# Performance work log

Hardware: AMD Instinct MI355X
Metric: run time of the kernel (lower is better)

## Reference

```python
import jax, jax.numpy as jnp
import numpy as np

N_NODES = 4096
N_EDGES = 16384
D_IN = 128
HID = 1024


def _linear_params(key, fan_in, fan_out):
    kw, kb = jax.random.split(key)
    bound = 1.0 / np.sqrt(fan_in)
    W = jax.random.uniform(kw, (fan_in, fan_out), jnp.float32, -bound, bound)
    b = jax.random.uniform(kb, (fan_out,), jnp.float32, -bound, bound)
    return W, b


def setup_inputs() -> dict:
    key = jax.random.key(0)
    ks = jax.random.split(key, 10)
    H = jax.random.normal(ks[0], (N_NODES, D_IN), jnp.float32)
    e = jax.random.uniform(ks[1], (N_NODES,), jnp.float32)
    # true incidence matrices: one-hot source/destination node per edge
    src = jax.random.randint(ks[2], (N_EDGES,), 0, N_NODES)
    dst = jax.random.randint(ks[3], (N_EDGES,), 0, N_NODES)
    Ro = jax.nn.one_hot(src, N_NODES, dtype=jnp.float32)  # [E, N]
    Ri = jax.nn.one_hot(dst, N_NODES, dtype=jnp.float32)  # [E, N]
    W1, b1 = _linear_params(ks[4], 3 * D_IN, HID)
    W2, b2 = _linear_params(ks[5], HID, HID)
    W3, b3 = _linear_params(ks[6], HID, HID // 2)
    W4, b4 = _linear_params(ks[7], HID // 2, HID // 4)
    W5, b5 = _linear_params(ks[8], HID // 4, 1)
    return {"H": H, "Ro": Ro, "Ri": Ri, "e": e,
            "W1": W1, "b1": b1, "W2": W2, "b2": b2, "W3": W3, "b3": b3,
            "W4": W4, "b4": b4, "W5": W5, "b5": b5}


def reference(H, Ro, Ri, e, W1, b1, W2, b2, W3, b3, W4, b4, W5, b5):
    eH = e[:, None] * H                      # [N, D]
    Ho = Ri.T @ (Ro @ eH)                    # aggregate over edges -> [N, D]
    Hi = Ro.T @ (Ri @ eH)                    # [N, D]
    x = jnp.concatenate([Ho, H, Hi], axis=1)  # [N, 3D]
    x = jnp.tanh(x @ W1 + b1)
    x = jnp.tanh(x @ W2 + b2)
    x = jnp.tanh(x @ W3 + b3)
    x = jnp.tanh(x @ W4 + b4)
    return jax.nn.sigmoid(x @ W5 + b5)       # [N, 1]
```

## Files before the change

kernel.cpp:

```cpp
#include <hip/hip_runtime.h>
#include <hip/hip_bf16.h>
#include <math.h>

#define N_NODES 4096
#define N_EDGES 16384
#define D_IN 128
#define HID 1024

typedef short s8v __attribute__((ext_vector_type(8)));
typedef float f4v __attribute__((ext_vector_type(4)));

__device__ __forceinline__ unsigned short f2b(float v) {
    union { float f; unsigned int u; } c; c.f = v;
    unsigned int u = c.u + 0x7fffu + ((c.u >> 16) & 1u);
    return (unsigned short)(u >> 16);
}
__device__ __forceinline__ float b2f(unsigned short b) {
    union { unsigned int u; float f; } c; c.u = ((unsigned int)b) << 16;
    return c.f;
}
__device__ __forceinline__ void glds16(const unsigned short* g, unsigned short* l) {
    __builtin_amdgcn_global_load_lds(
        (const __attribute__((address_space(1))) void*)g,
        (__attribute__((address_space(3))) void*)l, 16, 0, 0);
}

__global__ void extract_scatter(const float* __restrict__ Ro, const float* __restrict__ Ri,
                                const float* __restrict__ H, const float* __restrict__ e,
                                float* __restrict__ xf) {
    int edge = (blockIdx.x * 256 + threadIdx.x) >> 6;
    int l = threadIdx.x & 63;
    const float4* ro4 = (const float4*)(Ro + (size_t)edge * N_NODES);
    const float4* ri4 = (const float4*)(Ri + (size_t)edge * N_NODES);
    int src = -1, dst = -1;
    for (int it = 0; it < 16; ++it) {
        if (src < 0) {
            float4 v = ro4[it * 64 + l];
            bool hit = (v.x != 0.0f) | (v.y != 0.0f) | (v.z != 0.0f) | (v.w != 0.0f);
            unsigned long long m = __ballot(hit);
            if (m) {
                int fl = __ffsll((long long)m) - 1;
                int idx = 0;
                if (hit) idx = (it * 64 + l) * 4 + (v.x != 0.0f ? 0 : v.y != 0.0f ? 1 : v.z != 0.0f ? 2 : 3);
                src = __shfl(idx, fl);
            }
        }
        if (dst < 0) {
            float4 v = ri4[it * 64 + l];
            bool hit = (v.x != 0.0f) | (v.y != 0.0f) | (v.z != 0.0f) | (v.w != 0.0f);
            unsigned long long m = __ballot(hit);
            if (m) {
                int fl = __ffsll((long long)m) - 1;
                int idx = 0;
                if (hit) idx = (it * 64 + l) * 4 + (v.x != 0.0f ? 0 : v.y != 0.0f ? 1 : v.z != 0.0f ? 2 : 3);
                dst = __shfl(idx, fl);
            }
        }
        if (src >= 0 && dst >= 0) break;
    }
    float es = e[src], ed = e[dst];
    if (l < 32) {
        int f = l * 4;
        float4 h = *(const float4*)(H + (size_t)src * 128 + f);
        float* o = xf + (size_t)dst * 256 + f;
        atomicAdd(o + 0, es * h.x); atomicAdd(o + 1, es * h.y);
        atomicAdd(o + 2, es * h.z); atomicAdd(o + 3, es * h.w);
    } else {
        int f = (l - 32) * 4;
        float4 h = *(const float4*)(H + (size_t)dst * 128 + f);
        float* o = xf + (size_t)src * 256 + 128 + f;
        atomicAdd(o + 0, ed * h.x); atomicAdd(o + 1, ed * h.y);
        atomicAdd(o + 2, ed * h.z); atomicAdd(o + 3, ed * h.w);
    }
}

__global__ void wtrans_all(const float* __restrict__ W1, unsigned short* __restrict__ wt1,
                           const float* __restrict__ W2, unsigned short* __restrict__ wt2,
                           const float* __restrict__ W3, unsigned short* __restrict__ wt3,
                           const float* __restrict__ W4, unsigned short* __restrict__ wt4,
                           const float* __restrict__ W5, unsigned short* __restrict__ wt5) {
    int b = blockIdx.x, t = threadIdx.x;
    const float* W; unsigned short* WT; int K, N, tb;
    if (b < 384)       { W = W1; WT = wt1; K = 384;  N = 1024; tb = b; }
    else if (b < 1408) { W = W2; WT = wt2; K = 1024; N = 1024; tb = b - 384; }
    else if (b < 1920) { W = W3; WT = wt3; K = 1024; N = 512;  tb = b - 1408; }
    else if (b < 2048) { W = W4; WT = wt4; K = 512;  N = 256;  tb = b - 1920; }
    else { wt5[t] = f2b(W5[t]); return; }

    __shared__ float tile[32][33];
    int ntx = N >> 5;
    int tk = tb / ntx, tn = tb - tk * ntx;
    int tr = t >> 5, tc = t & 31;
#pragma unroll
    for (int i = 0; i < 4; ++i)
        tile[tr + i * 8][tc] = W[(size_t)(tk * 32 + tr + i * 8) * N + tn * 32 + tc];
    __syncthreads();
#pragma unroll
    for (int i = 0; i < 4; ++i)
        WT[(size_t)(tn * 32 + tr + i * 8) * K + tk * 32 + tc] = f2b(tile[tc][tr + i * 8]);
}

#define L1_BM 128
#define L1_BN 64
__global__ __launch_bounds__(256)
void gemm1(const float* __restrict__ xf, const float* __restrict__ H,
           const unsigned short* __restrict__ BT, const float* __restrict__ bias,
           unsigned short* __restrict__ C) {
    constexpr int BK = 32, K = 384, N = HID;
    constexpr int MI = L1_BM / 32, NI = L1_BN / 32;
    __shared__ unsigned short As[L1_BM * BK];
    __shared__ unsigned short Bs[L1_BN * BK];
    int t = threadIdx.x;
    int l = t & 63, w = t >> 6;
    int wm = w >> 1, wn = w & 1;
    int q = l >> 4, r16 = l & 15;
    int m0 = blockIdx.y * L1_BM, n0 = blockIdx.x * L1_BN;

    f4v acc[MI][NI] = {};

    for (int k0 = 0; k0 < K; k0 += BK) {
        __syncthreads();
#pragma unroll
        for (int i = 0; i < 2; ++i) {
            int c = i * 256 + t;
            int row = c >> 2, ko = (c & 3) * 8;
            const float* sp;
            if (k0 < 128)      sp = xf + (size_t)(m0 + row) * 256 + k0 + ko;
            else if (k0 < 256) sp = H + (size_t)(m0 + row) * 128 + (k0 - 128) + ko;
            else               sp = xf + (size_t)(m0 + row) * 256 + (k0 - 128) + ko;
            float4 f0 = *(const float4*)sp, f1 = *(const float4*)(sp + 4);
            s8v pk;
            pk[0] = (short)f2b(f0.x); pk[1] = (short)f2b(f0.y);
            pk[2] = (short)f2b(f0.z); pk[3] = (short)f2b(f0.w);
            pk[4] = (short)f2b(f1.x); pk[5] = (short)f2b(f1.y);
            pk[6] = (short)f2b(f1.z); pk[7] = (short)f2b(f1.w);
            *(s8v*)&As[c * 8] = pk;
        }
        {
            int c = w * 64 + l;
            int row = c >> 2, ko = (c & 3) * 8;
            glds16(&BT[(size_t)(n0 + row) * K + k0 + ko], &Bs[c * 8]);
        }
        __syncthreads();
        s8v a[MI], b[NI];
#pragma unroll
        for (int mi = 0; mi < MI; ++mi)
            a[mi] = *(const s8v*)&As[(wm * (L1_BM / 2) + mi * 16 + r16) * BK + q * 8];
#pragma unroll
        for (int ni = 0; ni < NI; ++ni)
            b[ni] = *(const s8v*)&Bs[(wn * (L1_BN / 2) + ni * 16 + r16) * BK + q * 8];
#pragma unroll
        for (int mi = 0; mi < MI; ++mi)
#pragma unroll
            for (int ni = 0; ni < NI; ++ni)
                acc[mi][ni] = __builtin_amdgcn_mfma_f32_16x16x32_bf16(a[mi], b[ni], acc[mi][ni], 0, 0, 0);
    }
#pragma unroll
    for (int mi = 0; mi < MI; ++mi)
#pragma unroll
        for (int ni = 0; ni < NI; ++ni) {
            int col = n0 + wn * (L1_BN / 2) + ni * 16 + r16;
            float bv = bias[col];
#pragma unroll
            for (int r = 0; r < 4; ++r) {
                int row = m0 + wm * (L1_BM / 2) + mi * 16 + q * 4 + r;
                C[(size_t)row * N + col] = f2b(tanhf(acc[mi][ni][r] + bv));
            }
        }
}

template<int BM, int BN>
__global__ __launch_bounds__(256)
void gemm_tanh(const unsigned short* __restrict__ A, const unsigned short* __restrict__ BT,
               const float* __restrict__ bias, unsigned short* __restrict__ C,
               int M, int N, int K) {
    constexpr int BK = 32;
    constexpr int MI = BM / 32, NI = BN / 32;
    constexpr int AITER = BM / 64, BITER = BN / 64;
    __shared__ unsigned short As[BM * BK];
    __shared__ unsigned short Bs[BN * BK];
    int t = threadIdx.x;
    int l = t & 63, w = t >> 6;
    int wm = w >> 1, wn = w & 1;
    int q = l >> 4, r16 = l & 15;
    int m0 = blockIdx.y * BM, n0 = blockIdx.x * BN;

    f4v acc[MI][NI] = {};

    for (int k0 = 0; k0 < K; k0 += BK) {
        __syncthreads();
#pragma unroll
        for (int i = 0; i < AITER; ++i) {
            int c = (i * 4 + w) * 64 + l;
            int row = c >> 2, ko = (c & 3) * 8;
            glds16(&A[(size_t)(m0 + row) * K + k0 + ko], &As[c * 8]);
        }
#pragma unroll
        for (int i = 0; i < BITER; ++i) {
            int c = (i * 4 + w) * 64 + l;
            int row = c >> 2, ko = (c & 3) * 8;
            glds16(&BT[(size_t)(n0 + row) * K + k0 + ko], &Bs[c * 8]);
        }
        __syncthreads();
        s8v a[MI], b[NI];
#pragma unroll
        for (int mi = 0; mi < MI; ++mi)
            a[mi] = *(const s8v*)&As[(wm * (BM / 2) + mi * 16 + r16) * BK + q * 8];
#pragma unroll
        for (int ni = 0; ni < NI; ++ni)
            b[ni] = *(const s8v*)&Bs[(wn * (BN / 2) + ni * 16 + r16) * BK + q * 8];
#pragma unroll
        for (int mi = 0; mi < MI; ++mi)
#pragma unroll
            for (int ni = 0; ni < NI; ++ni)
                acc[mi][ni] = __builtin_amdgcn_mfma_f32_16x16x32_bf16(a[mi], b[ni], acc[mi][ni], 0, 0, 0);
    }
#pragma unroll
    for (int mi = 0; mi < MI; ++mi)
#pragma unroll
        for (int ni = 0; ni < NI; ++ni) {
            int col = n0 + wn * (BN / 2) + ni * 16 + r16;
            float bv = bias[col];
#pragma unroll
            for (int r = 0; r < 4; ++r) {
                int row = m0 + wm * (BM / 2) + mi * 16 + q * 4 + r;
                C[(size_t)row * N + col] = f2b(tanhf(acc[mi][ni][r] + bv));
            }
        }
}

__global__ void layer5(const unsigned short* __restrict__ h4, const unsigned short* __restrict__ w5,
                       const float* __restrict__ b5, float* __restrict__ out) {
    int row = blockIdx.x * 4 + (threadIdx.x >> 6);
    int l = threadIdx.x & 63;
    const ushort4 hv = *(const ushort4*)(h4 + (size_t)row * 256 + l * 4);
    const ushort4 wv = *(const ushort4*)(w5 + l * 4);
    float s = b2f(hv.x) * b2f(wv.x) + b2f(hv.y) * b2f(wv.y)
            + b2f(hv.z) * b2f(wv.z) + b2f(hv.w) * b2f(wv.w);
#pragma unroll
    for (int off = 32; off > 0; off >>= 1) s += __shfl_down(s, off);
    if (l == 0) out[row] = 1.0f / (1.0f + expf(-(s + b5[0])));
}

extern "C" void kernel_launch(void* const* d_in, const int* in_sizes, int n_in,
                              void* d_out, int out_size, void* d_ws, size_t ws_size,
                              hipStream_t stream) {
    const float* H  = (const float*)d_in[0];
    const float* Ro = (const float*)d_in[1];
    const float* Ri = (const float*)d_in[2];
    const float* e  = (const float*)d_in[3];
    const float* W1 = (const float*)d_in[4];  const float* b1 = (const float*)d_in[5];
    const float* W2 = (const float*)d_in[6];  const float* b2 = (const float*)d_in[7];
    const float* W3 = (const float*)d_in[8];  const float* b3 = (const float*)d_in[9];
    const float* W4 = (const float*)d_in[10]; const float* b4 = (const float*)d_in[11];
    const float* W5 = (const float*)d_in[12]; const float* b5 = (const float*)d_in[13];
    float* out = (float*)d_out;

    char* p = (char*)d_ws;
    auto alloc = [&](size_t bytes) -> void* {
        void* r = (void*)p;
        p += (bytes + 255) & ~(size_t)255;
        return r;
    };
    float* xf = (float*)alloc((size_t)N_NODES * 256 * 4);
    unsigned short* h1  = (unsigned short*)alloc((size_t)N_NODES * HID * 2);
    unsigned short* h2  = (unsigned short*)alloc((size_t)N_NODES * HID * 2);
    unsigned short* h3  = (unsigned short*)alloc((size_t)N_NODES * (HID / 2) * 2);
    unsigned short* h4  = (unsigned short*)alloc((size_t)N_NODES * (HID / 4) * 2);
    unsigned short* wt1 = (unsigned short*)alloc((size_t)HID * 384 * 2);
    unsigned short* wt2 = (unsigned short*)alloc((size_t)HID * HID * 2);
    unsigned short* wt3 = (unsigned short*)alloc((size_t)(HID / 2) * HID * 2);
    unsigned short* wt4 = (unsigned short*)alloc((size_t)(HID / 4) * (HID / 2) * 2);
    unsigned short* wt5 = (unsigned short*)alloc((size_t)(HID / 4) * 2);

    hipMemsetAsync(xf, 0, (size_t)N_NODES * 256 * 4, stream);

    extract_scatter<<<N_EDGES / 4, 256, 0, stream>>>(Ro, Ri, H, e, xf);

    wtrans_all<<<2049, 256, 0, stream>>>(W1, wt1, W2, wt2, W3, wt3, W4, wt4, W5, wt5);

    gemm1<<<dim3(HID / L1_BN, N_NODES / L1_BM), 256, 0, stream>>>(xf, H, wt1, b1, h1);
    gemm_tanh<128, 64><<<dim3(HID / 64, N_NODES / 128), 256, 0, stream>>>(h1, wt2, b2, h2, N_NODES, HID, HID);
    gemm_tanh<64, 64><<<dim3((HID / 2) / 64, N_NODES / 64), 256, 0, stream>>>(h2, wt3, b3, h3, N_NODES, HID / 2, HID);
    gemm_tanh<64, 64><<<dim3((HID / 4) / 64, N_NODES / 64), 256, 0, stream>>>(h3, wt4, b4, h4, N_NODES, HID / 4, HID / 2);

    layer5<<<N_NODES / 4, 256, 0, stream>>>(h4, wt5, b5, out);
}
```

Baseline: 576.9 us.

## Fuse layers 4 and 5, fold xf zeroing into weight transpose, nontemporal scans

Replaces the layer-4 GEMM plus the separate layer-5 dot-product kernel with one kernel. Each block computes a full 256-wide row slice of layer 4, applies tanh and multiplies by W5 in registers, then reduces to the sigmoid output, so the h4 buffer is never written or re-read. The memset of the scatter buffer is merged into the weight-transpose launch, and the one-hot incidence matrix scans use nontemporal loads so they do not pollute cache. The cost is 128 blocks of 32 rows for the fused GEMM, which gives low parallelism, and each block reloads all of W4.

```diff
diff --git a/kernel.cpp b/kernel.cpp
--- a/kernel.cpp
+++ b/kernel.cpp
@@ -30,12 +30,12 @@
                                 float* __restrict__ xf) {
     int edge = (blockIdx.x * 256 + threadIdx.x) >> 6;
     int l = threadIdx.x & 63;
-    const float4* ro4 = (const float4*)(Ro + (size_t)edge * N_NODES);
-    const float4* ri4 = (const float4*)(Ri + (size_t)edge * N_NODES);
+    const f4v* ro4 = (const f4v*)(Ro + (size_t)edge * N_NODES);
+    const f4v* ri4 = (const f4v*)(Ri + (size_t)edge * N_NODES);
     int src = -1, dst = -1;
     for (int it = 0; it < 16; ++it) {
         if (src < 0) {
-            float4 v = ro4[it * 64 + l];
+            f4v v = __builtin_nontemporal_load(&ro4[it * 64 + l]);
             bool hit = (v.x != 0.0f) | (v.y != 0.0f) | (v.z != 0.0f) | (v.w != 0.0f);
             unsigned long long m = __ballot(hit);
             if (m) {
@@ -46,7 +46,7 @@
             }
         }
         if (dst < 0) {
-            float4 v = ri4[it * 64 + l];
+            f4v v = __builtin_nontemporal_load(&ri4[it * 64 + l]);
             bool hit = (v.x != 0.0f) | (v.y != 0.0f) | (v.z != 0.0f) | (v.w != 0.0f);
             unsigned long long m = __ballot(hit);
             if (m) {
@@ -74,18 +74,23 @@
     }
 }
 
-__global__ void wtrans_all(const float* __restrict__ W1, unsigned short* __restrict__ wt1,
-                           const float* __restrict__ W2, unsigned short* __restrict__ wt2,
-                           const float* __restrict__ W3, unsigned short* __restrict__ wt3,
-                           const float* __restrict__ W4, unsigned short* __restrict__ wt4,
-                           const float* __restrict__ W5, unsigned short* __restrict__ wt5) {
+__global__ void wtrans_zero(const float* __restrict__ W1, unsigned short* __restrict__ wt1,
+                            const float* __restrict__ W2, unsigned short* __restrict__ wt2,
+                            const float* __restrict__ W3, unsigned short* __restrict__ wt3,
+                            const float* __restrict__ W4, unsigned short* __restrict__ wt4,
+                            float* __restrict__ xf) {
     int b = blockIdx.x, t = threadIdx.x;
+    if (b >= 2048) {
+        float4 z = {0.f, 0.f, 0.f, 0.f};
+        float4* o = (float4*)(xf + (size_t)(b - 2048) * 2048) + t;
+        o[0] = z; o[256] = z;
+        return;
+    }
     const float* W; unsigned short* WT; int K, N, tb;
     if (b < 384)       { W = W1; WT = wt1; K = 384;  N = 1024; tb = b; }
     else if (b < 1408) { W = W2; WT = wt2; K = 1024; N = 1024; tb = b - 384; }
     else if (b < 1920) { W = W3; WT = wt3; K = 1024; N = 512;  tb = b - 1408; }
-    else if (b < 2048) { W = W4; WT = wt4; K = 512;  N = 256;  tb = b - 1920; }
-    else { wt5[t] = f2b(W5[t]); return; }
+    else               { W = W4; WT = wt4; K = 512;  N = 256;  tb = b - 1920; }
 
     __shared__ float tile[32][33];
     int ntx = N >> 5;
@@ -229,17 +234,70 @@
         }
 }
 
-__global__ void layer5(const unsigned short* __restrict__ h4, const unsigned short* __restrict__ w5,
-                       const float* __restrict__ b5, float* __restrict__ out) {
-    int row = blockIdx.x * 4 + (threadIdx.x >> 6);
-    int l = threadIdx.x & 63;
-    const ushort4 hv = *(const ushort4*)(h4 + (size_t)row * 256 + l * 4);
-    const ushort4 wv = *(const ushort4*)(w5 + l * 4);
-    float s = b2f(hv.x) * b2f(wv.x) + b2f(hv.y) * b2f(wv.y)
-            + b2f(hv.z) * b2f(wv.z) + b2f(hv.w) * b2f(wv.w);
-#pragma unroll
-    for (int off = 32; off > 0; off >>= 1) s += __shfl_down(s, off);
-    if (l == 0) out[row] = 1.0f / (1.0f + expf(-(s + b5[0])));
+__global__ __launch_bounds__(256)
+void gemm45(const unsigned short* __restrict__ A, const unsigned short* __restrict__ BT,
+            const float* __restrict__ b4, const float* __restrict__ W5,
+            const float* __restrict__ b5, float* __restrict__ out) {
+    constexpr int BK = 32, K = 512, NN = 256;
+    constexpr int NI = 8;
+    __shared__ unsigned short As[32 * BK];
+    __shared__ unsigned short Bs[NN * BK];
+    __shared__ float part[32][2];
+    int t = threadIdx.x;
+    int l = t & 63, w = t >> 6;
+    int wm = w >> 1, wn = w & 1;
+    int q = l >> 4, r16 = l & 15;
+    int m0 = blockIdx.y * 32;
+
+    f4v acc[NI] = {};
+
+    for (int k0 = 0; k0 < K; k0 += BK) {
+        __syncthreads();
+        if (w < 2) {
+            int c = w * 64 + l;
+            int row = c >> 2, ko = (c & 3) * 8;
+            glds16(&A[(size_t)(m0 + row) * K + k0 + ko], &As[c * 8]);
+        }
+#pragma unroll
+        for (int i = 0; i < 4; ++i) {
+            int c = (i * 4 + w) * 64 + l;
+            int row = c >> 2, ko = (c & 3) * 8;
+            glds16(&BT[(size_t)row * K + k0 + ko], &Bs[c * 8]);
+        }
+        __syncthreads();
+        s8v a = *(const s8v*)&As[(wm * 16 + r16) * BK + q * 8];
+        s8v b[NI];
+#pragma unroll
+        for (int ni = 0; ni < NI; ++ni)
+            b[ni] = *(const s8v*)&Bs[(wn * 128 + ni * 16 + r16) * BK + q * 8];
+#pragma unroll
+        for (int ni = 0; ni < NI; ++ni)
+            acc[ni] = __builtin_amdgcn_mfma_f32_16x16x32_bf16(a, b[ni], acc[ni], 0, 0, 0);
+    }
+
+    float partial[4] = {0.f, 0.f, 0.f, 0.f};
+#pragma unroll
+    for (int ni = 0; ni < NI; ++ni) {
+        int col = wn * 128 + ni * 16 + r16;
+        float bv = b4[col], wv = W5[col];
+#pragma unroll
+        for (int r = 0; r < 4; ++r)
+            partial[r] += tanhf(acc[ni][r] + bv) * wv;
+    }
+#pragma unroll
+    for (int off = 1; off < 16; off <<= 1)
+#pragma unroll
+        for (int r = 0; r < 4; ++r)
+            partial[r] += __shfl_xor(partial[r], off);
+    if (r16 == 0)
+#pragma unroll
+        for (int r = 0; r < 4; ++r)
+            part[wm * 16 + q * 4 + r][wn] = partial[r];
+    __syncthreads();
+    if (t < 32) {
+        float s = part[t][0] + part[t][1] + b5[0];
+        out[m0 + t] = 1.0f / (1.0f + expf(-s));
+    }
 }
 
 extern "C" void kernel_launch(void* const* d_in, const int* in_sizes, int n_in,
@@ -266,23 +324,18 @@
     unsigned short* h1  = (unsigned short*)alloc((size_t)N_NODES * HID * 2);
     unsigned short* h2  = (unsigned short*)alloc((size_t)N_NODES * HID * 2);
     unsigned short* h3  = (unsigned short*)alloc((size_t)N_NODES * (HID / 2) * 2);
-    unsigned short* h4  = (unsigned short*)alloc((size_t)N_NODES * (HID / 4) * 2);
     unsigned short* wt1 = (unsigned short*)alloc((size_t)HID * 384 * 2);
     unsigned short* wt2 = (unsigned short*)alloc((size_t)HID * HID * 2);
     unsigned short* wt3 = (unsigned short*)alloc((size_t)(HID / 2) * HID * 2);
     unsigned short* wt4 = (unsigned short*)alloc((size_t)(HID / 4) * (HID / 2) * 2);
-    unsigned short* wt5 = (unsigned short*)alloc((size_t)(HID / 4) * 2);
-
-    hipMemsetAsync(xf, 0, (size_t)N_NODES * 256 * 4, stream);
+
+    wtrans_zero<<<2560, 256, 0, stream>>>(W1, wt1, W2, wt2, W3, wt3, W4, wt4, xf);
 
     extract_scatter<<<N_EDGES / 4, 256, 0, stream>>>(Ro, Ri, H, e, xf);
-
-    wtrans_all<<<2049, 256, 0, stream>>>(W1, wt1, W2, wt2, W3, wt3, W4, wt4, W5, wt5);
 
     gemm1<<<dim3(HID / L1_BN, N_NODES / L1_BM), 256, 0, stream>>>(xf, H, wt1, b1, h1);
     gemm_tanh<128, 64><<<dim3(HID / 64, N_NODES / 128), 256, 0, stream>>>(h1, wt2, b2, h2, N_NODES, HID, HID);
     gemm_tanh<64, 64><<<dim3((HID / 2) / 64, N_NODES / 64), 256, 0, stream>>>(h2, wt3, b3, h3, N_NODES, HID / 2, HID);
-    gemm_tanh<64, 64><<<dim3((HID / 4) / 64, N_NODES / 64), 256, 0, stream>>>(h3, wt4, b4, h4, N_NODES, HID / 4, HID / 2);
-
-    layer5<<<N_NODES / 4, 256, 0, stream>>>(h4, wt5, b5, out);
-}
+
+    gemm45<<<dim3(1, N_NODES / 32), 256, 0, stream>>>(h3, wt4, b4, W5, b5, out);
+}
```

New measurement: 569.7 us. Within noise of the previous version (-1.2%).
